# Kernel optimization log

Hardware: AMD Instinct MI355X
Metric: run time of the kernel (lower is better)

## Reference

```python
import jax, jax.numpy as jnp
import numpy as np

B, N, C = 8, 1024, 1024
H = 16
D = C // H  # head_dim = 64
SCALE = D ** -0.5


def setup_inputs() -> dict:
    key = jax.random.key(0)
    k1, k2, k3 = jax.random.split(key, 3)
    x = jax.random.normal(k1, (B, N, C), dtype=jnp.float32)
    w_qkv = jax.random.normal(k2, (3 * C, C), dtype=jnp.float32) * (C ** -0.5)
    w_proj = jax.random.normal(k3, (C, C), dtype=jnp.float32) * (C ** -0.5)
    b_proj = jnp.zeros((C,), dtype=jnp.float32)
    return {"x": x, "w_qkv": w_qkv, "w_proj": w_proj, "b_proj": b_proj}


def reference(x, w_qkv, w_proj, b_proj):
    Bx, Nx, Cx = x.shape
    # qkv: [B,N,3C] -> [3,B,H,N,D]
    qkv = jnp.einsum('bnc,oc->bno', x, w_qkv)
    qkv = qkv.reshape(Bx, Nx, 3, H, D).transpose(2, 0, 3, 1, 4)
    q, k, v = qkv[0], qkv[1], qkv[2]
    attn = jnp.einsum('bhnd,bhmd->bhnm', q, k) * SCALE  # [B,H,N,N]
    attn = jax.nn.softmax(attn, axis=-1)
    out = jnp.einsum('bhnm,bhmd->bhnd', attn, v)  # [B,H,N,D]
    out = out.transpose(0, 2, 1, 3).reshape(Bx, Nx, Cx)
    return jnp.einsum('bnc,oc->bno', out, w_proj) + b_proj
```

## Files before the change

### kernel.cpp

```cpp
#include <hip/hip_runtime.h>

typedef _Float16 half8 __attribute__((ext_vector_type(8)));
typedef _Float16 half4v __attribute__((ext_vector_type(4)));
typedef _Float16 half2v __attribute__((ext_vector_type(2)));
typedef float floatx4 __attribute__((ext_vector_type(4)));

#define AS3 __attribute__((address_space(3)))
#define AS1 __attribute__((address_space(1)))

__device__ __forceinline__ void gload_lds16(const _Float16* g, _Float16* l) {
    __builtin_amdgcn_global_load_lds((AS1 void*)g, (AS3 void*)l, 16, 0, 0);
}

__device__ __forceinline__ floatx4 mfma16(half8 a, half8 b, floatx4 c) {
    return __builtin_amdgcn_mfma_f32_16x16x32_f16(a, b, c, 0, 0, 0);
}

__global__ __launch_bounds__(256) void cvt_all(const float* __restrict__ x,
                                               const float* __restrict__ wq,
                                               const float* __restrict__ wp,
                                               _Float16* __restrict__ xh,
                                               _Float16* __restrict__ wqh,
                                               _Float16* __restrict__ wph) {
    long i = (long)blockIdx.x * 256 + threadIdx.x;
    const float4* src; half4v* dst; long off;
    if (i < 2097152)      { src = (const float4*)x;  dst = (half4v*)xh;  off = i; }
    else if (i < 2883584) { src = (const float4*)wq; dst = (half4v*)wqh; off = i - 2097152; }
    else                  { src = (const float4*)wp; dst = (half4v*)wph; off = i - 2883584; }
    float4 v = src[off];
    half4v h = {(_Float16)v.x, (_Float16)v.y, (_Float16)v.z, (_Float16)v.w};
    dst[off] = h;
}

__global__ __launch_bounds__(512, 2) void gemm256(
    const _Float16* __restrict__ A, const _Float16* __restrict__ B,
    _Float16* __restrict__ Ch, int ldc, _Float16* __restrict__ Vt, int split,
    float* __restrict__ Cf, const float* __restrict__ bias, int Nn, int K)
{
    __shared__ _Float16 sAB[3 * 24576];

    const int nwg = gridDim.x * gridDim.y;
    int bid = blockIdx.y * gridDim.x + blockIdx.x;
    const int cpx = nwg >> 3;
    bid = (bid & 7) * cpx + (bid >> 3);
    const int gsz = gridDim.y << 3;
    const int bxg = bid / gsz;
    const int rem = bid - bxg * gsz;
    const int by = rem >> 3;
    const int bx = (bxg << 3) + (rem & 7);

    const int tid = threadIdx.x;
    const int lane = tid & 63, wave = tid >> 6;
    const int quad = lane >> 4, l16 = lane & 15;
    const int wm = wave >> 1, wn = wave & 1;
    const long m0 = (long)bx * 256, n0 = (long)by * 128;

    const int gch = ((tid & 7) ^ ((tid >> 3) & 7)) * 8;
    const _Float16* gA = A + (m0 + (tid >> 3)) * (long)K + gch;
    const _Float16* gB = B + (n0 + (tid >> 3)) * (long)K + gch;
    const int wst = wave * 512;

#define STAGE(sb, u) do {                                                     \
    const long ko = (long)(u) * 64;                                           \
    _Float16* d = &sAB[(sb) * 24576];                                         \
    gload_lds16(gA + ko,                 d + wst);                            \
    gload_lds16(gA +  64 * (long)K + ko, d + 4096  + wst);                    \
    gload_lds16(gA + 128 * (long)K + ko, d + 8192  + wst);                    \
    gload_lds16(gA + 192 * (long)K + ko, d + 12288 + wst);                    \
    gload_lds16(gB + ko,                 d + 16384 + wst);                    \
    gload_lds16(gB +  64 * (long)K + ko, d + 20480 + wst);                    \
} while (0)

    const int NT = K >> 6;
    STAGE(0, 0); STAGE(1, 1);
    asm volatile("s_waitcnt vmcnt(6)" ::: "memory");
    __builtin_amdgcn_s_barrier();

    const int cs0 = (quad ^ (l16 & 7)) * 8;
    const int cs1 = ((4 + quad) ^ (l16 & 7)) * 8;

    floatx4 acc[4][4] = {};
    half8 afr[4][2], bf0[2][2], bf1[2][2];

    int cb = 0, sb = 2;
    for (int t = 0; t < NT; ++t) {
        const _Float16* cA = &sAB[cb * 24576 + wm * 4096];
        const _Float16* cB = &sAB[cb * 24576 + 16384 + wn * 4096];

#pragma unroll
        for (int f = 0; f < 4; f++) {
            const _Float16* p = &cA[(f * 16 + l16) * 64];
            afr[f][0] = *(const half8*)&p[cs0];
            afr[f][1] = *(const half8*)&p[cs1];
        }
#pragma unroll
        for (int nf = 0; nf < 2; nf++) {
            const _Float16* p = &cB[(nf * 16 + l16) * 64];
            bf0[nf][0] = *(const half8*)&p[cs0];
            bf0[nf][1] = *(const half8*)&p[cs1];
        }
        if (t + 2 < NT) STAGE(sb, t + 2);
        __builtin_amdgcn_s_barrier();
        asm volatile("s_waitcnt lgkmcnt(0)" ::: "memory");
        __builtin_amdgcn_sched_barrier(0);
        __builtin_amdgcn_s_setprio(1);
#pragma unroll
        for (int f = 0; f < 4; f++)
#pragma unroll
            for (int nf = 0; nf < 2; nf++) {
                acc[f][nf] = mfma16(afr[f][0], bf0[nf][0], acc[f][nf]);
                acc[f][nf] = mfma16(afr[f][1], bf0[nf][1], acc[f][nf]);
            }
        __builtin_amdgcn_s_setprio(0);
        __builtin_amdgcn_s_barrier();

#pragma unroll
        for (int nf = 0; nf < 2; nf++) {
            const _Float16* p = &cB[((2 + nf) * 16 + l16) * 64];
            bf1[nf][0] = *(const half8*)&p[cs0];
            bf1[nf][1] = *(const half8*)&p[cs1];
        }
        __builtin_amdgcn_s_barrier();
        asm volatile("s_waitcnt lgkmcnt(0)" ::: "memory");
        __builtin_amdgcn_sched_barrier(0);
        __builtin_amdgcn_s_setprio(1);
#pragma unroll
        for (int f = 0; f < 4; f++)
#pragma unroll
            for (int nf = 0; nf < 2; nf++) {
                acc[f][2 + nf] = mfma16(afr[f][0], bf1[nf][0], acc[f][2 + nf]);
                acc[f][2 + nf] = mfma16(afr[f][1], bf1[nf][1], acc[f][2 + nf]);
            }
        __builtin_amdgcn_s_setprio(0);
        if (t + 2 < NT)       { asm volatile("s_waitcnt vmcnt(6)" ::: "memory"); }
        else if (t == NT - 2) { asm volatile("s_waitcnt vmcnt(0)" ::: "memory"); }
        __builtin_amdgcn_s_barrier();
        cb = (cb + 1 == 3) ? 0 : cb + 1;
        sb = (sb + 1 == 3) ? 0 : sb + 1;
    }
#undef STAGE

#pragma unroll
    for (int f = 0; f < 4; f++) {
        long row = m0 + wm * 64 + f * 16 + quad * 4;
#pragma unroll
        for (int cn = 0; cn < 4; cn++) {
            long col = n0 + wn * 64 + cn * 16 + l16;
            if (Cf) {
                float bv = bias ? bias[col] : 0.f;
#pragma unroll
                for (int r = 0; r < 4; r++)
                    Cf[(row + r) * (long)Nn + col] = acc[f][cn][r] + bv;
            } else if (col >= split) {
                long cv = col - split;
                long vrow = ((row >> 10) * 16 + (cv >> 6)) * 64 + (cv & 63);
                long nn = row & 1023;
                half4v pv = {(_Float16)acc[f][cn][0], (_Float16)acc[f][cn][1],
                             (_Float16)acc[f][cn][2], (_Float16)acc[f][cn][3]};
                *(half4v*)&Vt[vrow * 1024 + nn] = pv;
            } else {
#pragma unroll
                for (int r = 0; r < 4; r++)
                    Ch[(row + r) * (long)ldc + col] = (_Float16)acc[f][cn][r];
            }
        }
    }
}

#define CSC 0.125f
__global__ __launch_bounds__(256, 4) void flash_attn(const _Float16* __restrict__ qk,
                                                     const _Float16* __restrict__ vt,
                                                     _Float16* __restrict__ out)
{
    const int bh = blockIdx.x, b = bh >> 4, h = bh & 15;
    const int n0 = blockIdx.y * 128;
    const int tid = threadIdx.x, lane = tid & 63, wave = tid >> 6;
    const int quad = lane >> 4, l16 = lane & 15;

    __shared__ _Float16 sK[64 * 72];
    __shared__ _Float16 sVT[64 * 72];
    __shared__ _Float16 sPT[4][32 * 72];

    half8 qf[2][2];
    const _Float16* qbase = qk + (long)(b * 1024 + n0 + wave * 32) * 2048 + h * 64;
#pragma unroll
    for (int t = 0; t < 2; t++)
#pragma unroll
        for (int s = 0; s < 2; s++)
            qf[t][s] = *(const half8*)(qbase + (long)(t * 16 + l16) * 2048 + s * 32 + quad * 8);

    const int srow = tid >> 3, scol8 = (tid & 7) * 8;
    const _Float16* kgb = qk + 1024 + h * 64 + scol8 + (long)(b * 1024 + srow) * 2048;
    const _Float16* vgb = vt + (long)(bh * 64 + srow) * 1024 + scol8;

    float m_[2] = {-1e30f, -1e30f}, l_[2] = {0.f, 0.f};
    floatx4 o[2][4] = {};

    for (int kt = 0; kt < 16; kt++) {
        const int kr0 = kt * 64;
        __syncthreads();
#pragma unroll
        for (int i = 0; i < 2; i++) {
            int r = srow + i * 32;
            *(half8*)&sK[r * 72 + scol8]  = *(const half8*)(kgb + (long)(kr0 + i * 32) * 2048);
            *(half8*)&sVT[r * 72 + scol8] = *(const half8*)(vgb + (long)(i * 32) * 1024 + kr0);
        }
        __syncthreads();

        floatx4 sacc[2][4] = {};
#pragma unroll
        for (int c = 0; c < 4; c++)
#pragma unroll
            for (int s = 0; s < 2; s++) {
                half8 kf = *(const half8*)&sK[(c * 16 + l16) * 72 + s * 32 + quad * 8];
                sacc[0][c] = __builtin_amdgcn_mfma_f32_16x16x32_f16(kf, qf[0][s], sacc[0][c], 0, 0, 0);
                sacc[1][c] = __builtin_amdgcn_mfma_f32_16x16x32_f16(kf, qf[1][s], sacc[1][c], 0, 0, 0);
            }

#pragma unroll
        for (int t = 0; t < 2; t++) {
            float mx = -1e30f;
#pragma unroll
            for (int c = 0; c < 4; c++)
#pragma unroll
                for (int r = 0; r < 4; r++) {
                    float v = sacc[t][c][r] * CSC;
                    sacc[t][c][r] = v;
                    mx = fmaxf(mx, v);
                }
            mx = fmaxf(mx, __shfl_xor(mx, 16));
            mx = fmaxf(mx, __shfl_xor(mx, 32));
            float mn = fmaxf(m_[t], mx);
            float al = __expf(m_[t] - mn);
            m_[t] = mn;
            float rs = 0.f;
#pragma unroll
            for (int c = 0; c < 4; c++)
#pragma unroll
                for (int r = 0; r < 4; r++) {
                    float p = __expf(sacc[t][c][r] - mn);
                    sacc[t][c][r] = p;
                    rs += p;
                }
            rs += __shfl_xor(rs, 16);
            rs += __shfl_xor(rs, 32);
            l_[t] = l_[t] * al + rs;
#pragma unroll
            for (int dt = 0; dt < 4; dt++) o[t][dt] *= al;
#pragma unroll
            for (int c = 0; c < 4; c++) {
                half4v p = {(_Float16)sacc[t][c][0], (_Float16)sacc[t][c][1],
                            (_Float16)sacc[t][c][2], (_Float16)sacc[t][c][3]};
                *(half4v*)&sPT[wave][(t * 16 + l16) * 72 + c * 16 + quad * 4] = p;
            }
        }

#pragma unroll
        for (int kk = 0; kk < 2; kk++) {
            half8 pf0 = *(const half8*)&sPT[wave][(l16) * 72 + kk * 32 + quad * 8];
            half8 pf1 = *(const half8*)&sPT[wave][(16 + l16) * 72 + kk * 32 + quad * 8];
#pragma unroll
            for (int dt = 0; dt < 4; dt++) {
                half8 vf = *(const half8*)&sVT[(dt * 16 + l16) * 72 + kk * 32 + quad * 8];
                o[0][dt] = __builtin_amdgcn_mfma_f32_16x16x32_f16(vf, pf0, o[0][dt], 0, 0, 0);
                o[1][dt] = __builtin_amdgcn_mfma_f32_16x16x32_f16(vf, pf1, o[1][dt], 0, 0, 0);
            }
        }
    }

#pragma unroll
    for (int t = 0; t < 2; t++) {
        float inv = 1.f / l_[t];
#pragma unroll
        for (int dt = 0; dt < 4; dt++) {
            floatx4 v = o[t][dt];
            half4v a = {(_Float16)(v[0] * inv), (_Float16)(v[1] * inv),
                        (_Float16)(v[2] * inv), (_Float16)(v[3] * inv)};
            *(half4v*)&sPT[wave][(t * 16 + l16) * 72 + dt * 16 + quad * 4] = a;
        }
    }
    __syncthreads();
#pragma unroll
    for (int i = 0; i < 4; i++) {
        int ql = i * 8 + (lane >> 3);
        int c8 = (lane & 7) * 8;
        half8 vv = *(const half8*)&sPT[wave][ql * 72 + c8];
        *(half8*)(out + (long)(b * 1024 + n0 + wave * 32 + ql) * 1024 + h * 64 + c8) = vv;
    }
}

extern "C" void kernel_launch(void* const* d_in, const int* in_sizes, int n_in,
                              void* d_out, int out_size, void* d_ws, size_t ws_size,
                              hipStream_t stream) {
    const float* x      = (const float*)d_in[0];
    const float* w_qkv  = (const float*)d_in[1];
    const float* w_proj = (const float*)d_in[2];
    const float* b_proj = (const float*)d_in[3];

    char* ws = (char*)d_ws;
    _Float16* qkh    = (_Float16*)ws;
    _Float16* vT     = (_Float16*)(ws + 33554432);
    _Float16* xh     = (_Float16*)(ws + 50331648);
    _Float16* wqkvh  = (_Float16*)(ws + 67108864);
    _Float16* wprojh = (_Float16*)(ws + 73400320);
    _Float16* attnh  = xh;

    cvt_all<<<12288, 256, 0, stream>>>(x, w_qkv, w_proj, xh, wqkvh, wprojh);

    gemm256<<<dim3(32, 24), 512, 0, stream>>>(xh, wqkvh, qkh, 2048, vT, 2048,
                                              nullptr, nullptr, 3072, 1024);
    flash_attn<<<dim3(128, 8), 256, 0, stream>>>(qkh, vT, attnh);
    gemm256<<<dim3(32, 8), 512, 0, stream>>>(attnh, wprojh, nullptr, 0, nullptr, 1 << 30,
                                             (float*)d_out, b_proj, 1024, 1024);
}
```

Baseline: 236.1 us.

## Add 128x128 register-prefetch QKV GEMM and streamline flash attention softmax

Adds a new 128x128-tile GEMM kernel with swizzled LDS, register prefetch and double buffering, and uses it for the QKV projection in place of the 256-tile kernel. In flash attention, Q is pre-scaled by 1/sqrt(d) in fp16, K/V tiles are prefetched into registers one iteration ahead, and rescaling of the running max is skipped unless the max grows by more than a threshold. The lazy rescale lets exponent values reach up to e^8 before renormalisation, which is safe only because accumulation is in fp32; the pre-scaling in fp16 adds a small rounding change.

```diff
diff --git a/kernel.cpp b/kernel.cpp
--- a/kernel.cpp
+++ b/kernel.cpp
@@ -32,6 +32,100 @@
     dst[off] = h;
 }
 
+__global__ __launch_bounds__(256, 4) void gemm_tn(
+    const _Float16* __restrict__ A, const _Float16* __restrict__ B,
+    _Float16* __restrict__ Ch, int ldc, _Float16* __restrict__ Vt, int split,
+    float* __restrict__ Cf, const float* __restrict__ bias,
+    int M, int Nn, int K)
+{
+    __shared__ _Float16 sA[2][128 * 32];
+    __shared__ _Float16 sB[2][128 * 32];
+    const int tid  = threadIdx.x;
+    const int lane = tid & 63, wave = tid >> 6;
+    const int quad = lane >> 4, l16 = lane & 15;
+    const int wr = wave >> 1, wc = wave & 1;
+    const long m0 = (long)blockIdx.x * 128, n0 = (long)blockIdx.y * 128;
+
+    const int srow = tid >> 2;
+    const int sslot = ((tid & 3) ^ ((srow >> 1) & 3)) * 8;
+    const int dlo = srow * 32 + sslot;
+    const int dhi = (srow + 64) * 32 + sslot;
+    const _Float16* gA0 = A + (m0 + srow) * (long)K + (tid & 3) * 8;
+    const _Float16* gA1 = A + (m0 + srow + 64) * (long)K + (tid & 3) * 8;
+    const _Float16* gB0 = B + (n0 + srow) * (long)K + (tid & 3) * 8;
+    const _Float16* gB1 = B + (n0 + srow + 64) * (long)K + (tid & 3) * 8;
+
+    const int swz = (l16 >> 1) & 3;
+    const int aoff = ((quad ^ swz) * 8);
+
+    floatx4 acc[4][4] = {};
+    const int nk = K >> 5;
+
+    half8 rA0 = *(const half8*)gA0, rA1 = *(const half8*)gA1;
+    half8 rB0 = *(const half8*)gB0, rB1 = *(const half8*)gB1;
+    *(half8*)&sA[0][dlo] = rA0; *(half8*)&sA[0][dhi] = rA1;
+    *(half8*)&sB[0][dlo] = rB0; *(half8*)&sB[0][dhi] = rB1;
+
+    for (int kk = 0; kk < nk; kk++) {
+        const int cur = kk & 1;
+        __syncthreads();
+        const bool more = (kk + 1 < nk);
+        if (more) {
+            const long k0 = (long)(kk + 1) << 5;
+            rA0 = *(const half8*)(gA0 + k0); rA1 = *(const half8*)(gA1 + k0);
+            rB0 = *(const half8*)(gB0 + k0); rB1 = *(const half8*)(gB1 + k0);
+        }
+
+        const _Float16* cA = &sA[cur][0];
+        const _Float16* cB = &sB[cur][0];
+        half8 af[4], bf[4];
+#pragma unroll
+        for (int t = 0; t < 4; t++)
+            af[t] = *(const half8*)&cA[(wr * 64 + t * 16 + l16) * 32 + aoff];
+#pragma unroll
+        for (int t = 0; t < 4; t++)
+            bf[t] = *(const half8*)&cB[(wc * 64 + t * 16 + l16) * 32 + aoff];
+#pragma unroll
+        for (int tm = 0; tm < 4; tm++)
+#pragma unroll
+            for (int tn = 0; tn < 4; tn++)
+                acc[tm][tn] = __builtin_amdgcn_mfma_f32_16x16x32_f16(af[tm], bf[tn], acc[tm][tn], 0, 0, 0);
+
+        if (more) {
+            _Float16* nA = &sA[cur ^ 1][0];
+            _Float16* nB = &sB[cur ^ 1][0];
+            *(half8*)&nA[dlo] = rA0; *(half8*)&nA[dhi] = rA1;
+            *(half8*)&nB[dlo] = rB0; *(half8*)&nB[dhi] = rB1;
+        }
+    }
+
+#pragma unroll
+    for (int tm = 0; tm < 4; tm++) {
+        long row = m0 + wr * 64 + tm * 16 + quad * 4;
+#pragma unroll
+        for (int tn = 0; tn < 4; tn++) {
+            long col = n0 + wc * 64 + tn * 16 + l16;
+            if (Cf) {
+                float bv = bias ? bias[col] : 0.f;
+#pragma unroll
+                for (int r = 0; r < 4; r++)
+                    Cf[(row + r) * (long)Nn + col] = acc[tm][tn][r] + bv;
+            } else if (col >= split) {
+                long cv = col - split;
+                long vrow = ((row >> 10) * 16 + (cv >> 6)) * 64 + (cv & 63);
+                long nn = row & 1023;
+                half4v pv = {(_Float16)acc[tm][tn][0], (_Float16)acc[tm][tn][1],
+                             (_Float16)acc[tm][tn][2], (_Float16)acc[tm][tn][3]};
+                *(half4v*)&Vt[vrow * 1024 + nn] = pv;
+            } else {
+#pragma unroll
+                for (int r = 0; r < 4; r++)
+                    Ch[(row + r) * (long)ldc + col] = (_Float16)acc[tm][tn][r];
+            }
+        }
+    }
+}
+
 __global__ __launch_bounds__(512, 2) void gemm256(
     const _Float16* __restrict__ A, const _Float16* __restrict__ B,
     _Float16* __restrict__ Ch, int ldc, _Float16* __restrict__ Vt, int split,
@@ -167,7 +261,6 @@
     }
 }
 
-#define CSC 0.125f
 __global__ __launch_bounds__(256, 4) void flash_attn(const _Float16* __restrict__ qk,
                                                      const _Float16* __restrict__ vt,
                                                      _Float16* __restrict__ out)
@@ -186,8 +279,12 @@
 #pragma unroll
     for (int t = 0; t < 2; t++)
 #pragma unroll
-        for (int s = 0; s < 2; s++)
-            qf[t][s] = *(const half8*)(qbase + (long)(t * 16 + l16) * 2048 + s * 32 + quad * 8);
+        for (int s = 0; s < 2; s++) {
+            half8 v = *(const half8*)(qbase + (long)(t * 16 + l16) * 2048 + s * 32 + quad * 8);
+#pragma unroll
+            for (int j = 0; j < 8; j++) v[j] *= (_Float16)0.125f;
+            qf[t][s] = v;
+        }
 
     const int srow = tid >> 3, scol8 = (tid & 7) * 8;
     const _Float16* kgb = qk + 1024 + h * 64 + scol8 + (long)(b * 1024 + srow) * 2048;
@@ -196,16 +293,26 @@
     float m_[2] = {-1e30f, -1e30f}, l_[2] = {0.f, 0.f};
     floatx4 o[2][4] = {};
 
+    half8 rK0 = *(const half8*)(kgb);
+    half8 rK1 = *(const half8*)(kgb + (long)32 * 2048);
+    half8 rV0 = *(const half8*)(vgb);
+    half8 rV1 = *(const half8*)(vgb + (long)32 * 1024);
+
     for (int kt = 0; kt < 16; kt++) {
-        const int kr0 = kt * 64;
         __syncthreads();
-#pragma unroll
-        for (int i = 0; i < 2; i++) {
-            int r = srow + i * 32;
-            *(half8*)&sK[r * 72 + scol8]  = *(const half8*)(kgb + (long)(kr0 + i * 32) * 2048);
-            *(half8*)&sVT[r * 72 + scol8] = *(const half8*)(vgb + (long)(i * 32) * 1024 + kr0);
-        }
+        *(half8*)&sK[srow * 72 + scol8]          = rK0;
+        *(half8*)&sK[(srow + 32) * 72 + scol8]   = rK1;
+        *(half8*)&sVT[srow * 72 + scol8]         = rV0;
+        *(half8*)&sVT[(srow + 32) * 72 + scol8]  = rV1;
         __syncthreads();
+
+        if (kt + 1 < 16) {
+            const long kr0n = (long)(kt + 1) * 64;
+            rK0 = *(const half8*)(kgb + kr0n * 2048);
+            rK1 = *(const half8*)(kgb + (kr0n + 32) * 2048);
+            rV0 = *(const half8*)(vgb + kr0n);
+            rV1 = *(const half8*)(vgb + (long)32 * 1024 + kr0n);
+        }
 
         floatx4 sacc[2][4] = {};
 #pragma unroll
@@ -213,8 +320,8 @@
 #pragma unroll
             for (int s = 0; s < 2; s++) {
                 half8 kf = *(const half8*)&sK[(c * 16 + l16) * 72 + s * 32 + quad * 8];
-                sacc[0][c] = __builtin_amdgcn_mfma_f32_16x16x32_f16(kf, qf[0][s], sacc[0][c], 0, 0, 0);
-                sacc[1][c] = __builtin_amdgcn_mfma_f32_16x16x32_f16(kf, qf[1][s], sacc[1][c], 0, 0, 0);
+                sacc[0][c] = mfma16(kf, qf[0][s], sacc[0][c]);
+                sacc[1][c] = mfma16(kf, qf[1][s], sacc[1][c]);
             }
 
 #pragma unroll
@@ -223,30 +330,30 @@
 #pragma unroll
             for (int c = 0; c < 4; c++)
 #pragma unroll
-                for (int r = 0; r < 4; r++) {
-                    float v = sacc[t][c][r] * CSC;
-                    sacc[t][c][r] = v;
-                    mx = fmaxf(mx, v);
-                }
+                for (int r = 0; r < 4; r++)
+                    mx = fmaxf(mx, sacc[t][c][r]);
             mx = fmaxf(mx, __shfl_xor(mx, 16));
             mx = fmaxf(mx, __shfl_xor(mx, 32));
-            float mn = fmaxf(m_[t], mx);
-            float al = __expf(m_[t] - mn);
-            m_[t] = mn;
+            if (__any(mx > m_[t] + 8.f)) {
+                float mn = fmaxf(m_[t], mx);
+                float al = __expf(m_[t] - mn);
+                m_[t] = mn;
+                l_[t] *= al;
+#pragma unroll
+                for (int dt = 0; dt < 4; dt++) o[t][dt] *= al;
+            }
             float rs = 0.f;
 #pragma unroll
             for (int c = 0; c < 4; c++)
 #pragma unroll
                 for (int r = 0; r < 4; r++) {
-                    float p = __expf(sacc[t][c][r] - mn);
+                    float p = __expf(sacc[t][c][r] - m_[t]);
                     sacc[t][c][r] = p;
                     rs += p;
                 }
             rs += __shfl_xor(rs, 16);
             rs += __shfl_xor(rs, 32);
-            l_[t] = l_[t] * al + rs;
-#pragma unroll
-            for (int dt = 0; dt < 4; dt++) o[t][dt] *= al;
+            l_[t] += rs;
 #pragma unroll
             for (int c = 0; c < 4; c++) {
                 half4v p = {(_Float16)sacc[t][c][0], (_Float16)sacc[t][c][1],
@@ -262,8 +369,8 @@
 #pragma unroll
             for (int dt = 0; dt < 4; dt++) {
                 half8 vf = *(const half8*)&sVT[(dt * 16 + l16) * 72 + kk * 32 + quad * 8];
-                o[0][dt] = __builtin_amdgcn_mfma_f32_16x16x32_f16(vf, pf0, o[0][dt], 0, 0, 0);
-                o[1][dt] = __builtin_amdgcn_mfma_f32_16x16x32_f16(vf, pf1, o[1][dt], 0, 0, 0);
+                o[0][dt] = mfma16(vf, pf0, o[0][dt]);
+                o[1][dt] = mfma16(vf, pf1, o[1][dt]);
             }
         }
     }
@@ -307,8 +414,8 @@
 
     cvt_all<<<12288, 256, 0, stream>>>(x, w_qkv, w_proj, xh, wqkvh, wprojh);
 
-    gemm256<<<dim3(32, 24), 512, 0, stream>>>(xh, wqkvh, qkh, 2048, vT, 2048,
-                                              nullptr, nullptr, 3072, 1024);
+    gemm_tn<<<dim3(64, 24), 256, 0, stream>>>(xh, wqkvh, qkh, 2048, vT, 2048,
+                                              nullptr, nullptr, 8192, 3072, 1024);
     flash_attn<<<dim3(128, 8), 256, 0, stream>>>(qkh, vT, attnh);
     gemm256<<<dim3(32, 8), 512, 0, stream>>>(attnh, wprojh, nullptr, 0, nullptr, 1 << 30,
                                              (float*)d_out, b_proj, 1024, 1024);
```

Measured after the change: 243.3 us. +3.1%, slower.
